# Kernel optimization log

Measured on AMD Instinct MI355X. Metric: run time of the kernel, lower is better.

The kernel has to match this reference:

```python
import jax, jax.numpy as jnp
import numpy as np

N = 20480      # total nodes
E = 327680     # total edges (avg degree 16)
B = 16         # graphs in batch
IN = 16        # node feature dim
H = 8          # hidden_out_channel
CO = 64        # conv_out_channel
ET = 36        # n_edge_types
EF = 2         # edge_features
OUT = 1        # classifier out
DIMS = [(IN, H), (H, H), (H, H), (H, CO)]


def setup_inputs() -> dict:
    key = jax.random.key(0)
    ks = jax.random.split(key, 32)
    inp = {}
    inp['x'] = jax.random.normal(ks[0], (N, IN), jnp.float32)
    inp['edge_index'] = jax.random.randint(ks[1], (2, E), 0, N)
    inp['edge_type'] = jax.random.randint(ks[2], (E,), 0, ET)
    inp['edge_attr'] = jax.random.normal(ks[3], (E, EF), jnp.float32)
    inp['cell_type'] = jax.random.randint(ks[4], (N,), 0, 2)
    inp['batch'] = (jnp.arange(N) // (N // B)).astype(jnp.int32)
    i = 5
    for l, (ci, co) in enumerate(DIMS, 1):
        d = ci * co
        s = 1.0 / np.sqrt(EF)
        inp[f'emb{l}'] = jax.random.normal(ks[i], (ET, d), jnp.float32) * 0.02; i += 1
        inp[f'wh{l}'] = jax.random.normal(ks[i], (EF, d), jnp.float32) * s; i += 1
        inp[f'bh{l}'] = jnp.zeros((d,), jnp.float32)
        inp[f'wg{l}'] = jax.random.normal(ks[i], (EF, d), jnp.float32) * s; i += 1
        inp[f'bg{l}'] = jnp.zeros((d,), jnp.float32)
        inp[f'root{l}'] = jax.random.normal(ks[i], (ci, co), jnp.float32) / np.sqrt(ci); i += 1
        inp[f'bias{l}'] = jnp.zeros((co,), jnp.float32)
    inp['clf_w'] = jax.random.normal(ks[i], (CO, OUT), jnp.float32) / np.sqrt(CO)
    inp['clf_b'] = jnp.zeros((OUT,), jnp.float32)
    return inp


def edge_weights(etype, ef, emb, wh, bh, wg, bg):
    # EdgeNN: relu(embedding(type) * fc_h(feat) + fc_g(feat)) -> [E, cin*cout]
    return jax.nn.relu(emb[etype] * (ef @ wh + bh) + (ef @ wg + bg))


def nnconv(h, src, dst, W, root, bias):
    # NNConv(aggr='mean', root_weight=True): gather src feats, per-edge matmul, scatter-mean
    cin, cout = root.shape
    msg = jnp.einsum('ei,eio->eo', h[src], W.reshape(-1, cin, cout))  # [E, cout]
    agg = jax.ops.segment_sum(msg, dst, num_segments=N)
    deg = jax.ops.segment_sum(jnp.ones_like(msg[:, 0]), dst, num_segments=N)
    return agg / jnp.maximum(deg, 1.0)[:, None] + h @ root + bias


def reference(x, edge_index, edge_type, edge_attr, cell_type, batch,
              emb1, wh1, bh1, wg1, bg1, root1, bias1,
              emb2, wh2, bh2, wg2, bg2, root2, bias2,
              emb3, wh3, bh3, wg3, bg3, root3, bias3,
              emb4, wh4, bh4, wg4, bg4, root4, bias4,
              clf_w, clf_b):
    src, dst = edge_index[0], edge_index[1]
    layers = [(emb1, wh1, bh1, wg1, bg1, root1, bias1),
              (emb2, wh2, bh2, wg2, bg2, root2, bias2),
              (emb3, wh3, bh3, wg3, bg3, root3, bias3),
              (emb4, wh4, bh4, wg4, bg4, root4, bias4)]
    h = x
    for (emb, wh, bh, wg, bg, root, bias) in layers:  # fixed 4 structurally-distinct layers
        W = edge_weights(edge_type, edge_attr, emb, wh, bh, wg, bg)
        h = jax.nn.relu(nnconv(h, src, dst, W, root, bias))
    # gated scatter-mean pooling over tumor cells (cell_type == 1)
    gate = (cell_type == 1).astype(jnp.int32)
    seg = gate * (batch.astype(jnp.int32) + 1)  # 0 = masked-out bucket
    pooled = jax.ops.segment_sum(h, seg, num_segments=B + 1)
    cnt = jax.ops.segment_sum(jnp.ones((h.shape[0],), h.dtype), seg, num_segments=B + 1)
    pooled = (pooled / jnp.maximum(cnt, 1.0)[:, None])[1:B + 1]  # [B, CO]
    return jax.nn.sigmoid(pooled @ clf_w + clf_b)  # hazards [B, OUT]
```

## Files before the change

kernel.cpp:

```cpp
#include <hip/hip_runtime.h>
#include <math.h>

#define NN 20480
#define NE 327680
#define NBATCH 16

typedef float v2f __attribute__((ext_vector_type(2)));

static __device__ __forceinline__ v2f vmax0(v2f a) {
  v2f r; r.x = fmaxf(a.x, 0.f); r.y = fmaxf(a.y, 0.f); return r;
}
#define VMAX0 vmax0

__global__ __launch_bounds__(256) void prep_kernel(
    const int* __restrict__ dst, int* __restrict__ cnt,
    const float* __restrict__ e4, float* __restrict__ t4) {
  int b = blockIdx.x;
  if (b < NE / 256) {
    int e = b * 256 + threadIdx.x;
    atomicAdd(&cnt[dst[e]], 1);
  } else {
    int idx = (b - NE / 256) * 256 + threadIdx.x;
    int t = idx >> 9, rem = idx & 511;
    int q = rem >> 7, o = (rem >> 1) & 63, r = rem & 1;
    t4[idx] = e4[(t << 9) + (((q << 1) | r) << 6) + o];
  }
}

__global__ __launch_bounds__(1024) void scan_kernel(const int* __restrict__ cnt,
                                                    int* __restrict__ off,
                                                    int* __restrict__ cur,
                                                    float* __restrict__ poolz) {
  __shared__ int part[1024];
  int tid = threadIdx.x;
  if (tid < NBATCH * 64 + NBATCH) poolz[tid] = 0.f;
  const int PT = NN / 1024;
  int loc[PT];
  int run = 0;
  int base = tid * PT;
#pragma unroll
  for (int k = 0; k < PT; k++) { loc[k] = run; run += cnt[base + k]; }
  part[tid] = run;
  __syncthreads();
  for (int d = 1; d < 1024; d <<= 1) {
    int t = (tid >= d) ? part[tid - d] : 0;
    __syncthreads();
    part[tid] += t;
    __syncthreads();
  }
  int pre = (tid == 0) ? 0 : part[tid - 1];
#pragma unroll
  for (int k = 0; k < PT; k++) {
    off[base + k] = pre + loc[k];
    cur[base + k] = pre + loc[k];
  }
  if (tid == 1023) off[NN] = pre + run;
}

__global__ void scatter_kernel(const int* __restrict__ src, const int* __restrict__ dst,
                               const int* __restrict__ etype, const float* __restrict__ eattr,
                               int* __restrict__ cur, float4* __restrict__ es) {
  int e = blockIdx.x * blockDim.x + threadIdx.x;
  if (e >= NE) return;
  int d = dst[e];
  int pos = atomicAdd(&cur[d], 1);
  es[pos] = make_float4(__int_as_float(src[e]), __int_as_float(etype[e]),
                        eattr[2 * e], eattr[2 * e + 1]);
}

__global__ __launch_bounds__(256) void layer_small16(
    const int* __restrict__ off, const float4* __restrict__ es,
    const float* __restrict__ h_in,
    const float* __restrict__ emb, const float* __restrict__ wh,
    const float* __restrict__ bh, const float* __restrict__ wg,
    const float* __restrict__ bg,
    const float* __restrict__ root, const float* __restrict__ bias,
    float* __restrict__ h_out) {
  constexpr int D = 128;
  constexpr int S = D + 1;
  __shared__ float semb[36 * S];
  for (int idx = threadIdx.x; idx < 36 * D; idx += 256) {
    int t = idx / D, io = idx - t * D;
    semb[t * S + io] = emb[idx];
  }
  int lane = threadIdx.x & 63;
  int o = lane & 7;
  int ihalf = (lane >> 3) & 1;
  int esub = lane >> 4;
  int ibase = ihalf * 8;
  v2f rwh0[4], rwh1[4], rbh[4], rwg0[4], rwg1[4], rbg[4], rroot[4];
#pragma unroll
  for (int p = 0; p < 4; p++) {
    int a = (ibase + 2 * p) * 8 + o, b = (ibase + 2 * p + 1) * 8 + o;
    rwh0[p] = (v2f){wh[a], wh[b]};
    rwh1[p] = (v2f){wh[D + a], wh[D + b]};
    rbh[p]  = (v2f){bh[a], bh[b]};
    rwg0[p] = (v2f){wg[a], wg[b]};
    rwg1[p] = (v2f){wg[D + a], wg[D + b]};
    rbg[p]  = (v2f){bg[a], bg[b]};
    rroot[p] = (v2f){root[a], root[b]};
  }
  float rbias = bias[o];
  __syncthreads();
  int wid = __builtin_amdgcn_readfirstlane(blockIdx.x * 4 + (threadIdx.x >> 6));
  for (int k = 0; k < 2; k++) {
    int n = wid * 2 + k;
    int beg = off[n], end = off[n + 1];
    float acc = 0.f;
    for (int j = beg + esub; j < end; j += 4) {
      float4 rec = es[j];
      int s = __float_as_int(rec.x);
      int t = __float_as_int(rec.y);
      v2f ef0 = (v2f){rec.z, rec.z}, ef1 = (v2f){rec.w, rec.w};
      const float4* hp = (const float4*)(h_in + s * 16 + ibase);
      float4 h0 = hp[0], h1 = hp[1];
      v2f hv[4] = {(v2f){h0.x, h0.y}, (v2f){h0.z, h0.w},
                   (v2f){h1.x, h1.y}, (v2f){h1.z, h1.w}};
      const float* st = &semb[t * S + ibase * 8 + o];
      v2f msg = {0.f, 0.f};
#pragma unroll
      for (int p = 0; p < 4; p++) {
        v2f hval = rbh[p] + ef0 * rwh0[p] + ef1 * rwh1[p];
        v2f gval = rbg[p] + ef0 * rwg0[p] + ef1 * rwg1[p];
        v2f stv = (v2f){st[(2 * p) * 8], st[(2 * p + 1) * 8]};
        msg += hv[p] * VMAX0(stv * hval + gval);
      }
      acc += msg.x + msg.y;
    }
    acc += __shfl_xor(acc, 8);
    acc += __shfl_xor(acc, 16);
    acc += __shfl_xor(acc, 32);
    const float* hn = h_in + n * 16 + ibase;
    v2f rtv = {0.f, 0.f};
#pragma unroll
    for (int p = 0; p < 4; p++)
      rtv += (v2f){hn[2 * p], hn[2 * p + 1]} * rroot[p];
    float rt = rtv.x + rtv.y;
    rt += __shfl_xor(rt, 8);
    float deg = (float)(end - beg);
    float val = fmaxf(rbias + rt + acc / fmaxf(deg, 1.f), 0.f);
    if (lane < 8) h_out[n * 8 + o] = val;
  }
}

__global__ __launch_bounds__(256) void layer_small8(
    const int* __restrict__ off, const float4* __restrict__ es,
    const float* __restrict__ h_in,
    const float* __restrict__ emb, const float* __restrict__ wh,
    const float* __restrict__ bh, const float* __restrict__ wg,
    const float* __restrict__ bg,
    const float* __restrict__ root, const float* __restrict__ bias,
    float* __restrict__ h_out) {
  constexpr int D = 64;
  constexpr int S = D + 1;
  __shared__ float semb[36 * S];
  for (int idx = threadIdx.x; idx < 36 * D; idx += 256) {
    int t = idx / D, io = idx - t * D;
    semb[t * S + io] = emb[idx];
  }
  int lane = threadIdx.x & 63;
  int o = lane & 7, esub = lane >> 3;
  v2f rwh0[4], rwh1[4], rbh[4], rwg0[4], rwg1[4], rbg[4], rroot[4];
#pragma unroll
  for (int p = 0; p < 4; p++) {
    int a = (2 * p) * 8 + o, b = (2 * p + 1) * 8 + o;
    rwh0[p] = (v2f){wh[a], wh[b]};
    rwh1[p] = (v2f){wh[D + a], wh[D + b]};
    rbh[p]  = (v2f){bh[a], bh[b]};
    rwg0[p] = (v2f){wg[a], wg[b]};
    rwg1[p] = (v2f){wg[D + a], wg[D + b]};
    rbg[p]  = (v2f){bg[a], bg[b]};
    rroot[p] = (v2f){root[a], root[b]};
  }
  float rbias = bias[o];
  __syncthreads();
  int wid = __builtin_amdgcn_readfirstlane(blockIdx.x * 4 + (threadIdx.x >> 6));
  for (int k = 0; k < 4; k++) {
    int n = wid * 4 + k;
    int beg = off[n], end = off[n + 1];
    float acc = 0.f;
    for (int j = beg + esub; j < end; j += 8) {
      float4 rec = es[j];
      int s = __float_as_int(rec.x);
      int t = __float_as_int(rec.y);
      v2f ef0 = (v2f){rec.z, rec.z}, ef1 = (v2f){rec.w, rec.w};
      const float4* hp = (const float4*)(h_in + s * 8);
      float4 h0 = hp[0], h1 = hp[1];
      v2f hv[4] = {(v2f){h0.x, h0.y}, (v2f){h0.z, h0.w},
                   (v2f){h1.x, h1.y}, (v2f){h1.z, h1.w}};
      const float* st = &semb[t * S + o];
      v2f msg = {0.f, 0.f};
#pragma unroll
      for (int p = 0; p < 4; p++) {
        v2f hval = rbh[p] + ef0 * rwh0[p] + ef1 * rwh1[p];
        v2f gval = rbg[p] + ef0 * rwg0[p] + ef1 * rwg1[p];
        v2f stv = (v2f){st[(2 * p) * 8], st[(2 * p + 1) * 8]};
        msg += hv[p] * VMAX0(stv * hval + gval);
      }
      acc += msg.x + msg.y;
    }
    acc += __shfl_xor(acc, 8);
    acc += __shfl_xor(acc, 16);
    acc += __shfl_xor(acc, 32);
    float deg = (float)(end - beg);
    const float* hn = h_in + n * 8;
    v2f rtv = {0.f, 0.f};
#pragma unroll
    for (int p = 0; p < 4; p++)
      rtv += (v2f){hn[2 * p], hn[2 * p + 1]} * rroot[p];
    float val = fmaxf(rbias + rtv.x + rtv.y + acc / fmaxf(deg, 1.f), 0.f);
    if (lane < 8) h_out[n * 8 + o] = val;
  }
}

__global__ __launch_bounds__(512) void layer_l4(
    const int* __restrict__ off, const float4* __restrict__ es,
    const float* __restrict__ h_in, const float* __restrict__ embT,
    const float* __restrict__ wh, const float* __restrict__ bh,
    const float* __restrict__ wg, const float* __restrict__ bg,
    const float* __restrict__ root, const float* __restrict__ bias,
    float* __restrict__ h_out) {
  __shared__ float semb[36 * 512];
  for (int idx = threadIdx.x; idx < 36 * 128; idx += 512)
    ((float4*)semb)[idx] = ((const float4*)embT)[idx];
  int lane = threadIdx.x & 63;
  v2f rwh0[4], rwh1[4], rbh[4], rwg0[4], rwg1[4], rbg[4], rroot[4];
#pragma unroll
  for (int p = 0; p < 4; p++) {
    int a = (2 * p) * 64 + lane, b = (2 * p + 1) * 64 + lane;
    rwh0[p] = (v2f){wh[a], wh[b]};
    rwh1[p] = (v2f){wh[512 + a], wh[512 + b]};
    rbh[p]  = (v2f){bh[a], bh[b]};
    rwg0[p] = (v2f){wg[a], wg[b]};
    rwg1[p] = (v2f){wg[512 + a], wg[512 + b]};
    rbg[p]  = (v2f){bg[a], bg[b]};
    rroot[p] = (v2f){root[a], root[b]};
  }
  float rbias = bias[lane];
  __syncthreads();
  int base = __builtin_amdgcn_readfirstlane(
      (int)(blockIdx.x * 40) + (int)(threadIdx.x >> 6) * 5);
  const float* sl = &semb[lane * 2];
  for (int k = 0; k < 5; k++) {
    int n = base + k;
    int beg = off[n], end = off[n + 1];
    float acc0 = 0.f, acc1 = 0.f;
    int e = beg;
    for (; e + 2 <= end; e += 2) {
      float4 r0 = es[e], r1 = es[e + 1];
      int s0 = __float_as_int(r0.x), t0 = __float_as_int(r0.y);
      int s1 = __float_as_int(r1.x), t1 = __float_as_int(r1.y);
      const float4* hp0 = (const float4*)(h_in + s0 * 8);
      const float4* hp1 = (const float4*)(h_in + s1 * 8);
      float4 a0 = hp0[0], a1 = hp0[1];
      float4 b0 = hp1[0], b1 = hp1[1];
      const float* st0 = sl + t0 * 512;
      const float* st1 = sl + t1 * 512;
      v2f sv0[4], sv1[4];
#pragma unroll
      for (int q = 0; q < 4; q++) {
        sv0[q] = *(const v2f*)(st0 + q * 128);
        sv1[q] = *(const v2f*)(st1 + q * 128);
      }
      v2f hva[4] = {(v2f){a0.x, a0.y}, (v2f){a0.z, a0.w},
                    (v2f){a1.x, a1.y}, (v2f){a1.z, a1.w}};
      v2f hvb[4] = {(v2f){b0.x, b0.y}, (v2f){b0.z, b0.w},
                    (v2f){b1.x, b1.y}, (v2f){b1.z, b1.w}};
      v2f e00 = (v2f){r0.z, r0.z}, e01 = (v2f){r0.w, r0.w};
      v2f e10 = (v2f){r1.z, r1.z}, e11 = (v2f){r1.w, r1.w};
      v2f m0 = {0.f, 0.f}, m1 = {0.f, 0.f};
#pragma unroll
      for (int p = 0; p < 4; p++) {
        v2f hv0 = rbh[p] + e00 * rwh0[p] + e01 * rwh1[p];
        v2f gv0 = rbg[p] + e00 * rwg0[p] + e01 * rwg1[p];
        m0 += hva[p] * VMAX0(sv0[p] * hv0 + gv0);
        v2f hv1 = rbh[p] + e10 * rwh0[p] + e11 * rwh1[p];
        v2f gv1 = rbg[p] + e10 * rwg0[p] + e11 * rwg1[p];
        m1 += hvb[p] * VMAX0(sv1[p] * hv1 + gv1);
      }
      acc0 += m0.x + m0.y;
      acc1 += m1.x + m1.y;
    }
    if (e < end) {
      float4 r0 = es[e];
      int s0 = __float_as_int(r0.x), t0 = __float_as_int(r0.y);
      const float4* hp0 = (const float4*)(h_in + s0 * 8);
      float4 a0 = hp0[0], a1 = hp0[1];
      const float* st0 = sl + t0 * 512;
      v2f sv0[4];
#pragma unroll
      for (int q = 0; q < 4; q++) sv0[q] = *(const v2f*)(st0 + q * 128);
      v2f hva[4] = {(v2f){a0.x, a0.y}, (v2f){a0.z, a0.w},
                    (v2f){a1.x, a1.y}, (v2f){a1.z, a1.w}};
      v2f e00 = (v2f){r0.z, r0.z}, e01 = (v2f){r0.w, r0.w};
      v2f m0 = {0.f, 0.f};
#pragma unroll
      for (int p = 0; p < 4; p++) {
        v2f hv0 = rbh[p] + e00 * rwh0[p] + e01 * rwh1[p];
        v2f gv0 = rbg[p] + e00 * rwg0[p] + e01 * rwg1[p];
        m0 += hva[p] * VMAX0(sv0[p] * hv0 + gv0);
      }
      acc0 += m0.x + m0.y;
    }
    float acc = acc0 + acc1;
    float deg = (float)(end - beg);
    const float* hn = h_in + n * 8;
    v2f rtv = {0.f, 0.f};
#pragma unroll
    for (int p = 0; p < 4; p++)
      rtv += (v2f){hn[2 * p], hn[2 * p + 1]} * rroot[p];
    h_out[n * 64 + lane] = fmaxf(rbias + rtv.x + rtv.y + acc / fmaxf(deg, 1.f), 0.f);
  }
}

__global__ __launch_bounds__(256) void pool1_kernel(
    const float* __restrict__ h4, const int* __restrict__ ct,
    float* __restrict__ pooled, float* __restrict__ pcnt) {
  __shared__ float ss[4][64];
  __shared__ float sc[4];
  int b = blockIdx.x / 20, c = blockIdx.x % 20;
  int base = b * (NN / NBATCH) + c * 64;
  int o = threadIdx.x & 63, sub = threadIdx.x >> 6;
  float sum = 0.f, cnt = 0.f;
  for (int j = sub; j < 64; j += 4) {
    int n = base + j;
    if (ct[n] == 1) { sum += h4[n * 64 + o]; cnt += 1.f; }
  }
  ss[sub][o] = sum;
  if (o == 0) sc[sub] = cnt;
  __syncthreads();
  if (threadIdx.x < 64) {
    float tot = ss[0][o] + ss[1][o] + ss[2][o] + ss[3][o];
    unsafeAtomicAdd(&pooled[b * 64 + o], tot);
    if (o == 0) unsafeAtomicAdd(&pcnt[b], sc[0] + sc[1] + sc[2] + sc[3]);
  }
}

__global__ __launch_bounds__(1024) void pool2_kernel(
    const float* __restrict__ pooled, const float* __restrict__ pcnt,
    const float* __restrict__ clf_w, const float* __restrict__ clf_b,
    float* __restrict__ out) {
  int b = threadIdx.x >> 6, o = threadIdx.x & 63;
  float c = pcnt[b];
  float v = (pooled[b * 64 + o] / fmaxf(c, 1.f)) * clf_w[o];
#pragma unroll
  for (int d = 32; d; d >>= 1) v += __shfl_down(v, d);
  if (o == 0) out[b] = 1.f / (1.f + expf(-(v + clf_b[0])));
}

extern "C" void kernel_launch(void* const* d_in, const int* in_sizes, int n_in,
                              void* d_out, int out_size, void* d_ws, size_t ws_size,
                              hipStream_t stream) {
  (void)in_sizes; (void)n_in; (void)out_size; (void)ws_size;
  const float* x     = (const float*)d_in[0];
  const int*   eidx  = (const int*)d_in[1];
  const int*   src   = eidx;
  const int*   dst   = eidx + NE;
  const int*   etype = (const int*)d_in[2];
  const float* eattr = (const float*)d_in[3];
  const int*   ct    = (const int*)d_in[4];
  const float *emb[4], *wh[4], *bh[4], *wg[4], *bg[4], *root[4], *bias[4];
  for (int l = 0; l < 4; l++) {
    int b0 = 6 + 7 * l;
    emb[l]  = (const float*)d_in[b0 + 0];
    wh[l]   = (const float*)d_in[b0 + 1];
    bh[l]   = (const float*)d_in[b0 + 2];
    wg[l]   = (const float*)d_in[b0 + 3];
    bg[l]   = (const float*)d_in[b0 + 4];
    root[l] = (const float*)d_in[b0 + 5];
    bias[l] = (const float*)d_in[b0 + 6];
  }
  const float* clf_w = (const float*)d_in[34];
  const float* clf_b = (const float*)d_in[35];
  float* outp = (float*)d_out;

  float* ws  = (float*)d_ws;
  int*    off    = (int*)ws;
  float4* es     = (float4*)(ws + 20484);
  float*  hA     = ws + 20484 + 4 * NE;
  float*  hB     = hA + 8 * NN;
  float*  h4     = hB + 8 * NN;
  float*  embT4  = h4 + 64 * NN;
  float*  pooled = embT4 + 36 * 512;
  float*  pcnt   = pooled + 16 * 64;
  int*    cnt    = (int*)h4;
  int*    cur    = cnt + NN;

  hipMemsetAsync(cnt, 0, NN * sizeof(int), stream);
  prep_kernel<<<NE / 256 + 72, 256, 0, stream>>>(dst, cnt, emb[3], embT4);
  scan_kernel<<<1, 1024, 0, stream>>>(cnt, off, cur, pooled);
  scatter_kernel<<<NE / 256, 256, 0, stream>>>(src, dst, etype, eattr, cur, es);

  layer_small16<<<2560, 256, 0, stream>>>(off, es, x,
      emb[0], wh[0], bh[0], wg[0], bg[0], root[0], bias[0], hA);
  layer_small8<<<1280, 256, 0, stream>>>(off, es, hA,
      emb[1], wh[1], bh[1], wg[1], bg[1], root[1], bias[1], hB);
  layer_small8<<<1280, 256, 0, stream>>>(off, es, hB,
      emb[2], wh[2], bh[2], wg[2], bg[2], root[2], bias[2], hA);
  layer_l4<<<NN / 40, 512, 0, stream>>>(off, es, hA, embT4,
      wh[3], bh[3], wg[3], bg[3], root[3], bias[3], h4);

  pool1_kernel<<<320, 256, 0, stream>>>(h4, ct, pooled, pcnt);
  pool2_kernel<<<1, 1024, 0, stream>>>(pooled, pcnt, clf_w, clf_b, outp);
}
```

Baseline: 292.4 us.

## Fuse gated pooling into layer-4 kernel and interleave two nodes per wave

Layer 4 now accumulates the gated per-graph pooling sums in shared memory and atomically adds them to the global pooled buffer, so the 64-wide h4 output is never written and the separate pool1 kernel is dropped. Each wave now handles two nodes, with their edge loops interleaved for ILP, instead of five nodes processed sequentially. The grid grows to 1280 blocks for more parallelism. The cost is that each block reloads the 72 KB embedding table into LDS, which happens more often with smaller blocks, and the pooling adds shared atomics.

```diff
diff --git a/kernel.cpp b/kernel.cpp
--- a/kernel.cpp
+++ b/kernel.cpp
@@ -8,7 +8,7 @@
 typedef float v2f __attribute__((ext_vector_type(2)));
 
 static __device__ __forceinline__ v2f vmax0(v2f a) {
-  v2f r; r.x = fmaxf(a.x, 0.f); r.y = fmaxf(a.y, 0.f); return r;
+  return __builtin_elementwise_max(a, (v2f){0.f, 0.f});
 }
 #define VMAX0 vmax0
 
@@ -213,18 +213,48 @@
   }
 }
 
+static __device__ __forceinline__ void l4_edge(
+    const float4 r0, const float* __restrict__ h_in, const float* sl,
+    const v2f rwh0[4], const v2f rwh1[4], const v2f rbh[4],
+    const v2f rwg0[4], const v2f rwg1[4], const v2f rbg[4],
+    float& acc) {
+  int s0 = __float_as_int(r0.x), t0 = __float_as_int(r0.y);
+  const float4* hp0 = (const float4*)(h_in + s0 * 8);
+  float4 a0 = hp0[0], a1 = hp0[1];
+  const float* st0 = sl + t0 * 512;
+  v2f sv0[4];
+#pragma unroll
+  for (int q = 0; q < 4; q++) sv0[q] = *(const v2f*)(st0 + q * 128);
+  v2f hva[4] = {(v2f){a0.x, a0.y}, (v2f){a0.z, a0.w},
+                (v2f){a1.x, a1.y}, (v2f){a1.z, a1.w}};
+  v2f e00 = (v2f){r0.z, r0.z}, e01 = (v2f){r0.w, r0.w};
+  v2f m0 = {0.f, 0.f};
+#pragma unroll
+  for (int p = 0; p < 4; p++) {
+    v2f hv0 = rbh[p] + e00 * rwh0[p] + e01 * rwh1[p];
+    v2f gv0 = rbg[p] + e00 * rwg0[p] + e01 * rwg1[p];
+    m0 += hva[p] * VMAX0(sv0[p] * hv0 + gv0);
+  }
+  acc += m0.x + m0.y;
+}
+
 __global__ __launch_bounds__(512) void layer_l4(
     const int* __restrict__ off, const float4* __restrict__ es,
     const float* __restrict__ h_in, const float* __restrict__ embT,
     const float* __restrict__ wh, const float* __restrict__ bh,
     const float* __restrict__ wg, const float* __restrict__ bg,
     const float* __restrict__ root, const float* __restrict__ bias,
-    float* __restrict__ h_out) {
+    const int* __restrict__ ct,
+    float* __restrict__ pooled, float* __restrict__ pcnt) {
   __shared__ float semb[36 * 512];
+  __shared__ float sacc[64];
+  __shared__ float scnt;
   for (int idx = threadIdx.x; idx < 36 * 128; idx += 512)
     ((float4*)semb)[idx] = ((const float4*)embT)[idx];
+  if (threadIdx.x < 64) sacc[threadIdx.x] = 0.f;
+  if (threadIdx.x == 64) scnt = 0.f;
   int lane = threadIdx.x & 63;
-  v2f rwh0[4], rwh1[4], rbh[4], rwg0[4], rwg1[4], rbg[4], rroot[4];
+  v2f rwh0[4], rwh1[4], rbh[4], rwg0[4], rwg1[4], rbg[4];
 #pragma unroll
   for (int p = 0; p < 4; p++) {
     int a = (2 * p) * 64 + lane, b = (2 * p + 1) * 64 + lane;
@@ -234,106 +264,56 @@
     rwg0[p] = (v2f){wg[a], wg[b]};
     rwg1[p] = (v2f){wg[512 + a], wg[512 + b]};
     rbg[p]  = (v2f){bg[a], bg[b]};
-    rroot[p] = (v2f){root[a], root[b]};
   }
   float rbias = bias[lane];
   __syncthreads();
-  int base = __builtin_amdgcn_readfirstlane(
-      (int)(blockIdx.x * 40) + (int)(threadIdx.x >> 6) * 5);
+  int w = __builtin_amdgcn_readfirstlane((int)(threadIdx.x >> 6));
+  int nA = (int)blockIdx.x * 16 + w * 2;
+  int nB = nA + 1;
   const float* sl = &semb[lane * 2];
-  for (int k = 0; k < 5; k++) {
-    int n = base + k;
-    int beg = off[n], end = off[n + 1];
-    float acc0 = 0.f, acc1 = 0.f;
-    int e = beg;
-    for (; e + 2 <= end; e += 2) {
-      float4 r0 = es[e], r1 = es[e + 1];
-      int s0 = __float_as_int(r0.x), t0 = __float_as_int(r0.y);
-      int s1 = __float_as_int(r1.x), t1 = __float_as_int(r1.y);
-      const float4* hp0 = (const float4*)(h_in + s0 * 8);
-      const float4* hp1 = (const float4*)(h_in + s1 * 8);
-      float4 a0 = hp0[0], a1 = hp0[1];
-      float4 b0 = hp1[0], b1 = hp1[1];
-      const float* st0 = sl + t0 * 512;
-      const float* st1 = sl + t1 * 512;
-      v2f sv0[4], sv1[4];
-#pragma unroll
-      for (int q = 0; q < 4; q++) {
-        sv0[q] = *(const v2f*)(st0 + q * 128);
-        sv1[q] = *(const v2f*)(st1 + q * 128);
-      }
-      v2f hva[4] = {(v2f){a0.x, a0.y}, (v2f){a0.z, a0.w},
-                    (v2f){a1.x, a1.y}, (v2f){a1.z, a1.w}};
-      v2f hvb[4] = {(v2f){b0.x, b0.y}, (v2f){b0.z, b0.w},
-                    (v2f){b1.x, b1.y}, (v2f){b1.z, b1.w}};
-      v2f e00 = (v2f){r0.z, r0.z}, e01 = (v2f){r0.w, r0.w};
-      v2f e10 = (v2f){r1.z, r1.z}, e11 = (v2f){r1.w, r1.w};
-      v2f m0 = {0.f, 0.f}, m1 = {0.f, 0.f};
-#pragma unroll
-      for (int p = 0; p < 4; p++) {
-        v2f hv0 = rbh[p] + e00 * rwh0[p] + e01 * rwh1[p];
-        v2f gv0 = rbg[p] + e00 * rwg0[p] + e01 * rwg1[p];
-        m0 += hva[p] * VMAX0(sv0[p] * hv0 + gv0);
-        v2f hv1 = rbh[p] + e10 * rwh0[p] + e11 * rwh1[p];
-        v2f gv1 = rbg[p] + e10 * rwg0[p] + e11 * rwg1[p];
-        m1 += hvb[p] * VMAX0(sv1[p] * hv1 + gv1);
-      }
-      acc0 += m0.x + m0.y;
-      acc1 += m1.x + m1.y;
+  int begA = off[nA], endA = off[nA + 1];
+  int begB = off[nB], endB = off[nB + 1];
+  int degA = endA - begA, degB = endB - begB;
+  int cmn = degA < degB ? degA : degB;
+  float accA = 0.f, accB = 0.f;
+  for (int t = 0; t < cmn; ++t) {
+    float4 rA = es[begA + t];
+    float4 rB = es[begB + t];
+    l4_edge(rA, h_in, sl, rwh0, rwh1, rbh, rwg0, rwg1, rbg, accA);
+    l4_edge(rB, h_in, sl, rwh0, rwh1, rbh, rwg0, rwg1, rbg, accB);
+  }
+  for (int e = begA + cmn; e < endA; ++e) {
+    float4 r = es[e];
+    l4_edge(r, h_in, sl, rwh0, rwh1, rbh, rwg0, rwg1, rbg, accA);
+  }
+  for (int e = begB + cmn; e < endB; ++e) {
+    float4 r = es[e];
+    l4_edge(r, h_in, sl, rwh0, rwh1, rbh, rwg0, rwg1, rbg, accB);
+  }
+#pragma unroll 2
+  for (int which = 0; which < 2; ++which) {
+    int n = which ? nB : nA;
+    float acc = which ? accB : accA;
+    float deg = (float)(which ? degB : degA);
+    const float* hn = h_in + n * 8;
+    float rt = 0.f;
+#pragma unroll
+    for (int p = 0; p < 4; p++) {
+      v2f rr = (v2f){root[(2 * p) * 64 + lane], root[(2 * p + 1) * 64 + lane]};
+      rt += hn[2 * p] * rr.x + hn[2 * p + 1] * rr.y;
     }
-    if (e < end) {
-      float4 r0 = es[e];
-      int s0 = __float_as_int(r0.x), t0 = __float_as_int(r0.y);
-      const float4* hp0 = (const float4*)(h_in + s0 * 8);
-      float4 a0 = hp0[0], a1 = hp0[1];
-      const float* st0 = sl + t0 * 512;
-      v2f sv0[4];
-#pragma unroll
-      for (int q = 0; q < 4; q++) sv0[q] = *(const v2f*)(st0 + q * 128);
-      v2f hva[4] = {(v2f){a0.x, a0.y}, (v2f){a0.z, a0.w},
-                    (v2f){a1.x, a1.y}, (v2f){a1.z, a1.w}};
-      v2f e00 = (v2f){r0.z, r0.z}, e01 = (v2f){r0.w, r0.w};
-      v2f m0 = {0.f, 0.f};
-#pragma unroll
-      for (int p = 0; p < 4; p++) {
-        v2f hv0 = rbh[p] + e00 * rwh0[p] + e01 * rwh1[p];
-        v2f gv0 = rbg[p] + e00 * rwg0[p] + e01 * rwg1[p];
-        m0 += hva[p] * VMAX0(sv0[p] * hv0 + gv0);
-      }
-      acc0 += m0.x + m0.y;
+    float val = fmaxf(rbias + rt + acc / fmaxf(deg, 1.f), 0.f);
+    if (ct[n] == 1) {
+      atomicAdd(&sacc[lane], val);
+      if (lane == 0) atomicAdd(&scnt, 1.f);
     }
-    float acc = acc0 + acc1;
-    float deg = (float)(end - beg);
-    const float* hn = h_in + n * 8;
-    v2f rtv = {0.f, 0.f};
-#pragma unroll
-    for (int p = 0; p < 4; p++)
-      rtv += (v2f){hn[2 * p], hn[2 * p + 1]} * rroot[p];
-    h_out[n * 64 + lane] = fmaxf(rbias + rtv.x + rtv.y + acc / fmaxf(deg, 1.f), 0.f);
-  }
-}
-
-__global__ __launch_bounds__(256) void pool1_kernel(
-    const float* __restrict__ h4, const int* __restrict__ ct,
-    float* __restrict__ pooled, float* __restrict__ pcnt) {
-  __shared__ float ss[4][64];
-  __shared__ float sc[4];
-  int b = blockIdx.x / 20, c = blockIdx.x % 20;
-  int base = b * (NN / NBATCH) + c * 64;
-  int o = threadIdx.x & 63, sub = threadIdx.x >> 6;
-  float sum = 0.f, cnt = 0.f;
-  for (int j = sub; j < 64; j += 4) {
-    int n = base + j;
-    if (ct[n] == 1) { sum += h4[n * 64 + o]; cnt += 1.f; }
-  }
-  ss[sub][o] = sum;
-  if (o == 0) sc[sub] = cnt;
-  __syncthreads();
-  if (threadIdx.x < 64) {
-    float tot = ss[0][o] + ss[1][o] + ss[2][o] + ss[3][o];
-    unsafeAtomicAdd(&pooled[b * 64 + o], tot);
-    if (o == 0) unsafeAtomicAdd(&pcnt[b], sc[0] + sc[1] + sc[2] + sc[3]);
-  }
+  }
+  __syncthreads();
+  int bb = blockIdx.x / 80;
+  if (threadIdx.x < 64)
+    unsafeAtomicAdd(&pooled[bb * 64 + threadIdx.x], sacc[threadIdx.x]);
+  else if (threadIdx.x == 64)
+    unsafeAtomicAdd(&pcnt[bb], scnt);
 }
 
 __global__ __launch_bounds__(1024) void pool2_kernel(
@@ -379,11 +359,11 @@
   float4* es     = (float4*)(ws + 20484);
   float*  hA     = ws + 20484 + 4 * NE;
   float*  hB     = hA + 8 * NN;
-  float*  h4     = hB + 8 * NN;
-  float*  embT4  = h4 + 64 * NN;
+  float*  scratch= hB + 8 * NN;
+  float*  embT4  = scratch + 64 * NN;
   float*  pooled = embT4 + 36 * 512;
   float*  pcnt   = pooled + 16 * 64;
-  int*    cnt    = (int*)h4;
+  int*    cnt    = (int*)scratch;
   int*    cur    = cnt + NN;
 
   hipMemsetAsync(cnt, 0, NN * sizeof(int), stream);
@@ -397,9 +377,8 @@
       emb[1], wh[1], bh[1], wg[1], bg[1], root[1], bias[1], hB);
   layer_small8<<<1280, 256, 0, stream>>>(off, es, hB,
       emb[2], wh[2], bh[2], wg[2], bg[2], root[2], bias[2], hA);
-  layer_l4<<<NN / 40, 512, 0, stream>>>(off, es, hA, embT4,
-      wh[3], bh[3], wg[3], bg[3], root[3], bias[3], h4);
-
-  pool1_kernel<<<320, 256, 0, stream>>>(h4, ct, pooled, pcnt);
+  layer_l4<<<NN / 16, 512, 0, stream>>>(off, es, hA, embT4,
+      wh[3], bh[3], wg[3], bg[3], root[3], bias[3], ct, pooled, pcnt);
+
   pool2_kernel<<<1, 1024, 0, stream>>>(pooled, pcnt, clf_w, clf_b, outp);
 }
```

Measured after the change: 287.0 us. About the same (-1.8%).
